# Optimization experiments

Hardware: AMD Instinct MI355X
Metric: run time of the kernel (lower is better)

The kernel has to match this reference:

```python
import jax, jax.numpy as jnp
import numpy as np
from jax import lax

B_SZ, N_CH, N_T = 512, 129, 250
D_MODEL = 128
D_INNER = 256            # expand * d_model
D_STATE = 16
D_CONV = 4
HEADDIM = 64             # mamba_ssm default
NHEADS = D_INNER // HEADDIM  # 4
CONV_DIM = D_INNER + 2 * D_STATE        # 288 (ngroups=1)
D_IN_PROJ = 2 * D_INNER + 2 * D_STATE + NHEADS  # 548
EPS = 1e-5


def setup_inputs() -> dict:
    key = jax.random.key(0)
    ks = jax.random.split(key, 12)
    g = lambda k, shp, s: jax.random.normal(k, shp, jnp.float32) * s
    dt0 = jax.random.uniform(ks[4], (NHEADS,), minval=0.001, maxval=0.1)
    return {
        "x": jax.random.normal(ks[0], (B_SZ, N_CH, N_T), jnp.float32),
        "mixer_w": g(ks[1], (D_MODEL, N_CH), 0.05),
        "mixer_b": jnp.zeros((D_MODEL,), jnp.float32),
        "in_proj_w": g(ks[2], (D_IN_PROJ, D_MODEL), 0.05),
        "conv_w": g(ks[3], (CONV_DIM, D_CONV), 0.2),
        "conv_b": jnp.zeros((CONV_DIM,), jnp.float32),
        "dt_bias": jnp.log(jnp.expm1(dt0)),               # inverse-softplus init
        "A_log": jnp.log(jax.random.uniform(ks[5], (NHEADS,), minval=1.0, maxval=16.0)),
        "D": jnp.ones((NHEADS,), jnp.float32),
        "norm_w": jnp.ones((D_INNER,), jnp.float32),
        "out_proj_w": g(ks[6], (D_MODEL, D_INNER), 0.05),
        "head_w": g(ks[7], (1, D_MODEL), 0.05),
        "head_b": jnp.zeros((1,), jnp.float32),
    }


def reference(x, mixer_w, mixer_b, in_proj_w, conv_w, conv_b, dt_bias,
              A_log, D, norm_w, out_proj_w, head_w, head_b):
    bsz, _, T = x.shape
    # channel mixer: (B, C, T) -> (B, T, d_model)
    u = jnp.einsum('bct,dc->btd', x, mixer_w) + mixer_b
    # Mamba2 in_proj (no bias)
    zxbcdt = u @ in_proj_w.T                        # (B, T, 548)
    z = zxbcdt[..., :D_INNER]                       # gate
    xBC = zxbcdt[..., D_INNER:D_INNER + CONV_DIM]   # (B, T, 288)
    dt = jax.nn.softplus(zxbcdt[..., -NHEADS:] + dt_bias)  # (B, T, H)
    # causal depthwise conv1d (kernel 4) + SiLU
    pad = jnp.pad(xBC, ((0, 0), (D_CONV - 1, 0), (0, 0)))
    xBC = sum(conv_w[:, k] * pad[:, k:k + T, :] for k in range(D_CONV)) + conv_b
    xBC = jax.nn.silu(xBC)
    xh = xBC[..., :D_INNER].reshape(bsz, T, NHEADS, HEADDIM)
    Bm = xBC[..., D_INNER:D_INNER + D_STATE]        # (B, T, N)
    Cm = xBC[..., D_INNER + D_STATE:]               # (B, T, N)
    A = -jnp.exp(A_log)                             # (H,)
    dA = jnp.exp(dt * A)                            # (B, T, H)
    # selective state-space scan, time-major
    tm = lambda a: jnp.moveaxis(a, 1, 0)
    def step(h, inp):
        dA_t, dt_t, x_t, B_t, C_t = inp
        # h: (B, H, P, N)
        h = h * dA_t[:, :, None, None] + (dt_t[..., None] * x_t)[..., None] * B_t[:, None, None, :]
        y_t = jnp.einsum('bhpn,bn->bhp', h, C_t)
        return h, y_t
    h0 = jnp.zeros((bsz, NHEADS, HEADDIM, D_STATE), x.dtype)
    _, ys = lax.scan(step, h0, (tm(dA), tm(dt), tm(xh), tm(Bm), tm(Cm)))
    y = jnp.moveaxis(ys, 0, 1) + D[:, None] * xh    # skip connection, (B, T, H, P)
    y = y.reshape(bsz, T, D_INNER)
    # gated RMSNorm (norm_before_gate=False)
    y = y * jax.nn.silu(z)
    y = y * lax.rsqrt(jnp.mean(y * y, axis=-1, keepdims=True) + EPS) * norm_w
    y = y @ out_proj_w.T                            # (B, T, d_model)
    # head: AdaptiveAvgPool1d(1) over time -> Flatten -> Linear(d_model, 1)
    pooled = jnp.mean(y, axis=1)                    # (B, d_model)
    return pooled @ head_w.T + head_b               # (B, 1)
```

## Files before the change

kernel.cpp:

```cpp
#include <hip/hip_runtime.h>
#include <math.h>

#define NCH     129
#define NT      250
#define DINNER  256
#define DSTATE  16
#define NHEADS  4
#define DPROJ   548
#define TC      8
#define MT      35
#define KS4     4
#define ZR      17
#define XK      136

typedef __attribute__((ext_vector_type(8))) short short8;
typedef __attribute__((ext_vector_type(4))) float f32x4;

template<int N> struct IC { static constexpr int value = N; };

__device__ __forceinline__ float silu_f(float x) { return x / (1.f + __expf(-x)); }

template<int CTRL>
__device__ __forceinline__ float dstep(float v) {
    int t = __builtin_amdgcn_update_dpp(0, __float_as_int(v), CTRL, 0xF, 0xF, true);
    return v + __int_as_float(t);
}
__device__ __forceinline__ float wave_sum63(float v) {
    v = dstep<0xB1>(v);  v = dstep<0x4E>(v);  v = dstep<0x141>(v);
    v = dstep<0x140>(v); v = dstep<0x142>(v); v = dstep<0x143>(v);
    return v;
}
__device__ __forceinline__ float rdlane(float v, int l) {
    return __uint_as_float(__builtin_amdgcn_readlane(__float_as_uint(v), l));
}
__device__ __forceinline__ unsigned short f2bf(float f) {
    unsigned u = __float_as_uint(f);
    u += 0x7FFF + ((u >> 16) & 1);
    return (unsigned short)(u >> 16);
}
__device__ __forceinline__ float bf2f(unsigned short h) {
    return __uint_as_float(((unsigned)h) << 16);
}

__global__ __launch_bounds__(256) void k_prep_w2(const float* __restrict__ in_proj_w,
                                                 const float* __restrict__ mixer_w,
                                                 const float* __restrict__ mixer_b,
                                                 float* __restrict__ w2t,
                                                 float* __restrict__ bias2) {
    int j = blockIdx.x;
    int c = threadIdx.x;
    if (c < NCH) {
        float acc = 0.f;
        for (int d = 0; d < 128; ++d)
            acc += in_proj_w[j * 128 + d] * mixer_w[d * NCH + c];
        w2t[(size_t)c * DPROJ + j] = acc;
    } else if (c == NCH) {
        float acc = 0.f;
        for (int d = 0; d < 128; ++d)
            acc += in_proj_w[j * 128 + d] * mixer_b[d];
        bias2[j] = acc;
    }
}

__global__ __launch_bounds__(256) void k_prep_v(const float* __restrict__ head_w,
                                                const float* __restrict__ out_proj_w,
                                                float* __restrict__ v) {
    int i = threadIdx.x;
    float acc = 0.f;
    for (int d = 0; d < 128; ++d)
        acc += head_w[d] * out_proj_w[(size_t)d * DINNER + i];
    v[i] = acc;
}

__global__ __launch_bounds__(64) void k_prep_frag(const float* __restrict__ w2t,
                                                  unsigned short* __restrict__ ahi,
                                                  unsigned short* __restrict__ alo) {
    int mt = blockIdx.x, ks = blockIdx.y;
    int lane = threadIdx.x;
    int m = mt * 16 + (lane & 15);
    size_t base = (((size_t)(mt * KS4 + ks)) * 64 + lane) * 8;
    for (int i = 0; i < 8; ++i) {
        int k = ks * 32 + (lane >> 4) * 8 + i;
        float v = (m < DPROJ) ? w2t[(size_t)k * DPROJ + m] : 0.f;
        unsigned short hb = f2bf(v);
        ahi[base + i] = hb;
        alo[base + i] = f2bf(v - bf2f(hb));
    }
}

__global__ __launch_bounds__(640, 2) void k_fused(
    const float* __restrict__ x,
    const unsigned short* __restrict__ ahi,
    const unsigned short* __restrict__ alo,
    const float* __restrict__ w2t,
    const float* __restrict__ bias2,
    const float* __restrict__ conv_w,
    const float* __restrict__ conv_b,
    const float* __restrict__ dt_bias,
    const float* __restrict__ A_log,
    const float* __restrict__ Dv,
    const float* __restrict__ norm_w,
    const float* __restrict__ vv,
    const float* __restrict__ head_b,
    float* __restrict__ out)
{
    __shared__ short xh[16 * XK];
    __shared__ short xl[16 * XK];
    __shared__ float x128buf[2][2][TC];
    __shared__ float zxbuf[DPROJ * ZR];
    __shared__ float bcbuf[2][TC][32];
    __shared__ float dtbuf[2][TC][NHEADS];
    __shared__ float dAbuf[2][TC][NHEADS];
    __shared__ float smp[2][2][TC][8];

    const int b2   = blockIdx.x;
    const int tid  = threadIdx.x;
    const int lane = tid & 63;
    const int wv   = tid >> 6;
    const bool isMain = (wv < 8);
    const int mb   = isMain ? (wv >> 2) : (wv - 8);
    const int p    = ((wv & 3) << 6) | lane;
    const int q    = lane;
    const int tcol = lane & 15;
    const int quad = lane >> 4;
    const bool isFold = isMain && ((wv & 3) == 0);

    const float* w128 = w2t + (size_t)128 * DPROJ;

    float bz = 0.f, bx = 0.f, w1z = 0.f, w1x = 0.f;
    float cw0 = 0.f, cw1 = 0.f, cw2 = 0.f, cw3 = 0.f, ccb = 0.f;
    float dtb = 0.f, Ah = 0.f, Dh = 0.f, nv = 0.f;
    if (isMain) {
        bz = bias2[p];          w1z = w128[p];
        bx = bias2[DINNER + p]; w1x = w128[DINNER + p];
        cw0 = conv_w[p * 4 + 0]; cw1 = conv_w[p * 4 + 1];
        cw2 = conv_w[p * 4 + 2]; cw3 = conv_w[p * 4 + 3];
        ccb = conv_b[p];
        Dh = Dv[p >> 6];
        nv = norm_w[p] * vv[p];
    } else if (q < 36) {
        bx  = bias2[2 * DINNER + q];
        w1x = w128[2 * DINNER + q];
        if (q < 32) {
            int ch = DINNER + q;
            cw0 = conv_w[ch * 4 + 0]; cw1 = conv_w[ch * 4 + 1];
            cw2 = conv_w[ch * 4 + 2]; cw3 = conv_w[ch * 4 + 3];
            ccb = conv_b[ch];
        } else {
            int h = q - 32;
            dtb = dt_bias[h];
            Ah  = -expf(A_log[h]);
        }
    }

    float za[TC], xa[TC], hs[DSTATE];
    float c1 = 0.f, c2 = 0.f, c3 = 0.f, outacc = 0.f;
#pragma unroll
    for (int n = 0; n < DSTATE; ++n) hs[n] = 0.f;

    const float* xb_aux = x + ((size_t)2 * b2 + mb) * NCH * NT;
    const int hh = wv & 3;
    float2 pr[9];

    auto load_chunk = [&](int t0, auto Lc) {
        constexpr int L  = decltype(Lc)::value;
        constexpr int HP = (L >= 2) ? L / 2 : 1;
        constexpr int PAIRS = NCH * HP;
#pragma unroll
        for (int k = 0; k * 64 < PAIRS; ++k) {
            int u = lane + 64 * k;
            if (u < PAIRS) {
                int c = u / HP, tp = u - c * HP;
                pr[k] = *(const float2*)(xb_aux + c * NT + t0 + 2 * tp);
            }
        }
    };
    auto store_chunk = [&](auto Lc, int nxtpar) {
        constexpr int L  = decltype(Lc)::value;
        constexpr int HP = (L >= 2) ? L / 2 : 1;
        constexpr int PAIRS = NCH * HP;
#pragma unroll
        for (int k = 0; k * 64 < PAIRS; ++k) {
            int u = lane + 64 * k;
            if (u < PAIRS) {
                int c = u / HP, tp = u - c * HP;
                float2 v = pr[k];
                if (c < 128) {
                    int row = mb * 8 + 2 * tp;
                    unsigned short h0 = f2bf(v.x), h1 = f2bf(v.y);
                    xh[row * XK + c]       = (short)h0;
                    xh[(row + 1) * XK + c] = (short)h1;
                    xl[row * XK + c]       = (short)f2bf(v.x - bf2f(h0));
                    xl[(row + 1) * XK + c] = (short)f2bf(v.y - bf2f(h1));
                } else {
                    x128buf[nxtpar][mb][2 * tp]     = v.x;
                    x128buf[nxtpar][mb][2 * tp + 1] = v.y;
                }
            }
        }
    };

    if (!isMain) { load_chunk(0, IC<TC>{}); store_chunk(IC<TC>{}, 0); }
    __syncthreads();

    auto stage = [&](auto CLc, auto NLc, int s) {
        constexpr int CL = decltype(CLc)::value;
        constexpr int NL = decltype(NLc)::value;
        const int cur = s & 1;

        if (isMain) {
            short8 bh[KS4], bl[KS4];
#pragma unroll
            for (int ks = 0; ks < KS4; ++ks) {
                bh[ks] = *(const short8*)&xh[tcol * XK + ks * 32 + quad * 8];
                bl[ks] = *(const short8*)&xl[tcol * XK + ks * 32 + quad * 8];
            }
            for (int mt = wv; mt < MT; mt += 8) {
                f32x4 a0 = {0.f, 0.f, 0.f, 0.f};
                f32x4 a1 = {0.f, 0.f, 0.f, 0.f};
#pragma unroll
                for (int ks = 0; ks < KS4; ++ks) {
                    size_t fo = (((size_t)(mt * KS4 + ks)) * 64 + lane) * 8;
                    short8 ah = *(const short8*)(ahi + fo);
                    short8 al = *(const short8*)(alo + fo);
                    a0 = __builtin_amdgcn_mfma_f32_16x16x32_bf16(ah, bh[ks], a0, 0, 0, 0);
                    a1 = __builtin_amdgcn_mfma_f32_16x16x32_bf16(ah, bl[ks], a1, 0, 0, 0);
                    a1 = __builtin_amdgcn_mfma_f32_16x16x32_bf16(al, bh[ks], a1, 0, 0, 0);
                }
#pragma unroll
                for (int r = 0; r < 4; ++r) {
                    int j = mt * 16 + quad * 4 + r;
                    if (j < DPROJ) zxbuf[j * ZR + tcol] = a0[r] + a1[r];
                }
            }
        } else {
            if constexpr (NL > 0) load_chunk((s + 1) * TC, IC<NL>{});
        }
        __syncthreads();

        if (isMain) {
            if (isFold && s > 0 && lane < TC) {
                const float* sp = smp[(s - 1) & 1][mb][lane];
                float s1 = sp[0] + sp[2] + sp[4] + sp[6];
                float s2 = sp[1] + sp[3] + sp[5] + sp[7];
                outacc = fmaf(s2, rsqrtf(fmaf(s1, 1.f / DINNER, 1e-5f)), outacc);
            }
#pragma unroll
            for (int tt = 0; tt < CL; ++tt) {
                float xm = x128buf[cur][mb][tt];
                int col = mb * 8 + tt;
                float zraw = zxbuf[p * ZR + col] + bz + w1z * xm;
                float xraw = zxbuf[(DINNER + p) * ZR + col] + bx + w1x * xm;
                float cv = fmaf(cw3, xraw, fmaf(cw2, c1, fmaf(cw1, c2, fmaf(cw0, c3, ccb))));
                c3 = c2; c2 = c1; c1 = xraw;
                xa[tt] = silu_f(cv);
                za[tt] = silu_f(zraw);
            }
        } else {
            if constexpr (NL > 0) store_chunk(IC<NL>{}, (s + 1) & 1);
            if (q < 32) {
#pragma unroll
                for (int tt = 0; tt < CL; ++tt) {
                    float xm = x128buf[cur][mb][tt];
                    float raw = zxbuf[(2 * DINNER + q) * ZR + mb * 8 + tt] + bx + w1x * xm;
                    float cv = fmaf(cw3, raw, fmaf(cw2, c1, fmaf(cw1, c2, fmaf(cw0, c3, ccb))));
                    c3 = c2; c2 = c1; c1 = raw;
                    bcbuf[mb][tt][q] = silu_f(cv);
                }
            } else if (q < 36) {
                int h = q - 32;
#pragma unroll
                for (int tt = 0; tt < CL; ++tt) {
                    float xm = x128buf[cur][mb][tt];
                    float val = zxbuf[(544 + h) * ZR + mb * 8 + tt] + bx + w1x * xm + dtb;
                    float dt = (val > 20.f) ? val : log1pf(expf(val));
                    dtbuf[mb][tt][h] = dt;
                    dAbuf[mb][tt][h] = __expf(dt * Ah);
                }
            }
        }
        __syncthreads();

        if (isMain) {
#pragma unroll
            for (int tt = 0; tt < CL; ++tt) {
                float xv  = xa[tt];
                float g   = za[tt];
                float dtv = dtbuf[mb][tt][hh];
                float dAv = dAbuf[mb][tt][hh];
                float bcv = bcbuf[mb][tt][lane & 31];
                float dx = dtv * xv;
                float y0 = 0.f, y1 = 0.f, y2 = 0.f, y3 = 0.f;
#pragma unroll
                for (int n = 0; n < 4; ++n) {
                    float b0 = rdlane(bcv, n),      cc0 = rdlane(bcv, DSTATE + n);
                    float b1 = rdlane(bcv, 4 + n),  cc1 = rdlane(bcv, DSTATE + 4 + n);
                    float b2v = rdlane(bcv, 8 + n), cc2 = rdlane(bcv, DSTATE + 8 + n);
                    float b3 = rdlane(bcv, 12 + n), cc3 = rdlane(bcv, DSTATE + 12 + n);
                    hs[n]      = fmaf(hs[n],      dAv, dx * b0);  y0 = fmaf(hs[n],      cc0, y0);
                    hs[4 + n]  = fmaf(hs[4 + n],  dAv, dx * b1);  y1 = fmaf(hs[4 + n],  cc1, y1);
                    hs[8 + n]  = fmaf(hs[8 + n],  dAv, dx * b2v); y2 = fmaf(hs[8 + n],  cc2, y2);
                    hs[12 + n] = fmaf(hs[12 + n], dAv, dx * b3);  y3 = fmaf(hs[12 + n], cc3, y3);
                }
                float val = fmaf(Dh, xv, (y0 + y1) + (y2 + y3)) * g;
                float s1 = wave_sum63(val * val);
                float s2 = wave_sum63(val * nv);
                if (lane == 63) {
                    smp[cur][mb][tt][2 * (wv & 3)]     = s1;
                    smp[cur][mb][tt][2 * (wv & 3) + 1] = s2;
                }
            }
        }
    };

    stage(IC<8>{}, IC<8>{}, 0);
    for (int s = 1; s <= 29; ++s) stage(IC<8>{}, IC<8>{}, s);
    stage(IC<8>{}, IC<2>{}, 30);
    stage(IC<2>{}, IC<0>{}, 31);
    __syncthreads();

    if (isFold) {
        if (lane < 2) {
            const float* sp = smp[1][mb][lane];
            float s1 = sp[0] + sp[2] + sp[4] + sp[6];
            float s2 = sp[1] + sp[3] + sp[5] + sp[7];
            outacc = fmaf(s2, rsqrtf(fmaf(s1, 1.f / DINNER, 1e-5f)), outacc);
        }
        float tot = wave_sum63(outacc);
        if (lane == 63) out[2 * b2 + mb] = head_b[0] + tot * (1.f / NT);
    }
}

extern "C" void kernel_launch(void* const* d_in, const int* in_sizes, int n_in,
                              void* d_out, int out_size, void* d_ws, size_t ws_size,
                              hipStream_t stream) {
    const float* x         = (const float*)d_in[0];
    const float* mixer_w   = (const float*)d_in[1];
    const float* mixer_b   = (const float*)d_in[2];
    const float* in_proj_w = (const float*)d_in[3];
    const float* conv_w    = (const float*)d_in[4];
    const float* conv_b    = (const float*)d_in[5];
    const float* dt_bias   = (const float*)d_in[6];
    const float* A_log     = (const float*)d_in[7];
    const float* Dp        = (const float*)d_in[8];
    const float* norm_w    = (const float*)d_in[9];
    const float* out_proj_w= (const float*)d_in[10];
    const float* head_w    = (const float*)d_in[11];
    const float* head_b    = (const float*)d_in[12];
    float* out = (float*)d_out;

    int B = in_sizes[0] / (NCH * NT);

    float* ws    = (float*)d_ws;
    float* w2t   = ws;
    float* bias2 = w2t + (size_t)NCH * DPROJ;
    float* vvp   = bias2 + DPROJ;
    unsigned short* ahi = (unsigned short*)(vvp + DINNER);
    unsigned short* alo = ahi + (size_t)MT * KS4 * 64 * 8;

    k_prep_w2<<<DPROJ, 256, 0, stream>>>(in_proj_w, mixer_w, mixer_b, w2t, bias2);
    k_prep_v<<<1, 256, 0, stream>>>(head_w, out_proj_w, vvp);
    k_prep_frag<<<dim3(MT, KS4), 64, 0, stream>>>(w2t, ahi, alo);
    k_fused<<<B / 2, 640, 0, stream>>>(x, ahi, alo, w2t, bias2, conv_w, conv_b,
                                       dt_bias, A_log, Dp, norm_w, vvp, head_b, out);
}
```

Before: 428.4 us.

## Use one batch per block with 16-step time chunks and prefetched A fragments

Each block now handles one batch element with 5 waves (4 main, 1 loader) instead of two batch elements with 10 waves. The time chunk doubles to 16 steps, so all 16 MFMA columns hold real timesteps and there are half as many stage barriers. The A-fragment loads are double-buffered across M-tiles to hide global latency. In exchange there are twice as many blocks and more registers per thread (larger prefetch arrays and buffered fragments), which may limit occupancy.

```diff
diff --git a/kernel.cpp b/kernel.cpp
--- a/kernel.cpp
+++ b/kernel.cpp
@@ -7,7 +7,7 @@
 #define DSTATE  16
 #define NHEADS  4
 #define DPROJ   548
-#define TC      8
+#define TC      16
 #define MT      35
 #define KS4     4
 #define ZR      17
@@ -88,7 +88,7 @@
     }
 }
 
-__global__ __launch_bounds__(640, 2) void k_fused(
+__global__ __launch_bounds__(320, 3) void k_fused(
     const float* __restrict__ x,
     const unsigned short* __restrict__ ahi,
     const unsigned short* __restrict__ alo,
@@ -104,26 +104,25 @@
     const float* __restrict__ head_b,
     float* __restrict__ out)
 {
-    __shared__ short xh[16 * XK];
-    __shared__ short xl[16 * XK];
-    __shared__ float x128buf[2][2][TC];
+    __shared__ short xh[TC * XK];
+    __shared__ short xl[TC * XK];
+    __shared__ float x128buf[2][TC];
     __shared__ float zxbuf[DPROJ * ZR];
-    __shared__ float bcbuf[2][TC][32];
-    __shared__ float dtbuf[2][TC][NHEADS];
-    __shared__ float dAbuf[2][TC][NHEADS];
-    __shared__ float smp[2][2][TC][8];
-
-    const int b2   = blockIdx.x;
+    __shared__ float bcbuf[TC][32];
+    __shared__ float dtbuf[TC][NHEADS];
+    __shared__ float dAbuf[TC][NHEADS];
+    __shared__ float smp[2][TC][8];
+
+    const int b    = blockIdx.x;
     const int tid  = threadIdx.x;
     const int lane = tid & 63;
     const int wv   = tid >> 6;
-    const bool isMain = (wv < 8);
-    const int mb   = isMain ? (wv >> 2) : (wv - 8);
-    const int p    = ((wv & 3) << 6) | lane;
+    const bool isMain = (wv < 4);
+    const int p    = (wv << 6) | lane;
     const int q    = lane;
     const int tcol = lane & 15;
     const int quad = lane >> 4;
-    const bool isFold = isMain && ((wv & 3) == 0);
+    const bool isFold = (wv == 0);
 
     const float* w128 = w2t + (size_t)128 * DPROJ;
 
@@ -136,7 +135,7 @@
         cw0 = conv_w[p * 4 + 0]; cw1 = conv_w[p * 4 + 1];
         cw2 = conv_w[p * 4 + 2]; cw3 = conv_w[p * 4 + 3];
         ccb = conv_b[p];
-        Dh = Dv[p >> 6];
+        Dh = Dv[wv];
         nv = norm_w[p] * vv[p];
     } else if (q < 36) {
         bx  = bias2[2 * DINNER + q];
@@ -158,9 +157,8 @@
 #pragma unroll
     for (int n = 0; n < DSTATE; ++n) hs[n] = 0.f;
 
-    const float* xb_aux = x + ((size_t)2 * b2 + mb) * NCH * NT;
-    const int hh = wv & 3;
-    float2 pr[9];
+    const float* xb = x + (size_t)b * NCH * NT;
+    float2 pr[17];
 
     auto load_chunk = [&](int t0, auto Lc) {
         constexpr int L  = decltype(Lc)::value;
@@ -171,7 +169,7 @@
             int u = lane + 64 * k;
             if (u < PAIRS) {
                 int c = u / HP, tp = u - c * HP;
-                pr[k] = *(const float2*)(xb_aux + c * NT + t0 + 2 * tp);
+                pr[k] = *(const float2*)(xb + c * NT + t0 + 2 * tp);
             }
         }
     };
@@ -186,15 +184,15 @@
                 int c = u / HP, tp = u - c * HP;
                 float2 v = pr[k];
                 if (c < 128) {
-                    int row = mb * 8 + 2 * tp;
+                    int row = 2 * tp;
                     unsigned short h0 = f2bf(v.x), h1 = f2bf(v.y);
                     xh[row * XK + c]       = (short)h0;
                     xh[(row + 1) * XK + c] = (short)h1;
                     xl[row * XK + c]       = (short)f2bf(v.x - bf2f(h0));
                     xl[(row + 1) * XK + c] = (short)f2bf(v.y - bf2f(h1));
                 } else {
-                    x128buf[nxtpar][mb][2 * tp]     = v.x;
-                    x128buf[nxtpar][mb][2 * tp + 1] = v.y;
+                    x128buf[nxtpar][2 * tp]     = v.x;
+                    x128buf[nxtpar][2 * tp + 1] = v.y;
                 }
             }
         }
@@ -215,23 +213,41 @@
                 bh[ks] = *(const short8*)&xh[tcol * XK + ks * 32 + quad * 8];
                 bl[ks] = *(const short8*)&xl[tcol * XK + ks * 32 + quad * 8];
             }
-            for (int mt = wv; mt < MT; mt += 8) {
+            short8 f0h[KS4], f0l[KS4], f1h[KS4], f1l[KS4];
+            auto loadA = [&](int mt, short8 (&fh)[KS4], short8 (&fl)[KS4]) {
+#pragma unroll
+                for (int ks = 0; ks < KS4; ++ks) {
+                    size_t fo = (((size_t)(mt * KS4 + ks)) * 64 + lane) * 8;
+                    fh[ks] = *(const short8*)(ahi + fo);
+                    fl[ks] = *(const short8*)(alo + fo);
+                }
+            };
+            auto tileC = [&](int mt, short8 (&fh)[KS4], short8 (&fl)[KS4]) {
                 f32x4 a0 = {0.f, 0.f, 0.f, 0.f};
                 f32x4 a1 = {0.f, 0.f, 0.f, 0.f};
 #pragma unroll
                 for (int ks = 0; ks < KS4; ++ks) {
-                    size_t fo = (((size_t)(mt * KS4 + ks)) * 64 + lane) * 8;
-                    short8 ah = *(const short8*)(ahi + fo);
-                    short8 al = *(const short8*)(alo + fo);
-                    a0 = __builtin_amdgcn_mfma_f32_16x16x32_bf16(ah, bh[ks], a0, 0, 0, 0);
-                    a1 = __builtin_amdgcn_mfma_f32_16x16x32_bf16(ah, bl[ks], a1, 0, 0, 0);
-                    a1 = __builtin_amdgcn_mfma_f32_16x16x32_bf16(al, bh[ks], a1, 0, 0, 0);
+                    a0 = __builtin_amdgcn_mfma_f32_16x16x32_bf16(fh[ks], bh[ks], a0, 0, 0, 0);
+                    a1 = __builtin_amdgcn_mfma_f32_16x16x32_bf16(fh[ks], bl[ks], a1, 0, 0, 0);
+                    a1 = __builtin_amdgcn_mfma_f32_16x16x32_bf16(fl[ks], bh[ks], a1, 0, 0, 0);
                 }
 #pragma unroll
                 for (int r = 0; r < 4; ++r) {
                     int j = mt * 16 + quad * 4 + r;
                     if (j < DPROJ) zxbuf[j * ZR + tcol] = a0[r] + a1[r];
                 }
+            };
+            int mt = wv;
+            loadA(mt, f0h, f0l);
+            while (true) {
+                if (mt + 4 < MT) loadA(mt + 4, f1h, f1l);
+                tileC(mt, f0h, f0l);
+                mt += 4;
+                if (mt >= MT) break;
+                if (mt + 4 < MT) loadA(mt + 4, f0h, f0l);
+                tileC(mt, f1h, f1l);
+                mt += 4;
+                if (mt >= MT) break;
             }
         } else {
             if constexpr (NL > 0) load_chunk((s + 1) * TC, IC<NL>{});
@@ -240,17 +256,16 @@
 
         if (isMain) {
             if (isFold && s > 0 && lane < TC) {
-                const float* sp = smp[(s - 1) & 1][mb][lane];
+                const float* sp = smp[(s - 1) & 1][lane];
                 float s1 = sp[0] + sp[2] + sp[4] + sp[6];
                 float s2 = sp[1] + sp[3] + sp[5] + sp[7];
                 outacc = fmaf(s2, rsqrtf(fmaf(s1, 1.f / DINNER, 1e-5f)), outacc);
             }
 #pragma unroll
             for (int tt = 0; tt < CL; ++tt) {
-                float xm = x128buf[cur][mb][tt];
-                int col = mb * 8 + tt;
-                float zraw = zxbuf[p * ZR + col] + bz + w1z * xm;
-                float xraw = zxbuf[(DINNER + p) * ZR + col] + bx + w1x * xm;
+                float xm = x128buf[cur][tt];
+                float zraw = zxbuf[p * ZR + tt] + bz + w1z * xm;
+                float xraw = zxbuf[(DINNER + p) * ZR + tt] + bx + w1x * xm;
                 float cv = fmaf(cw3, xraw, fmaf(cw2, c1, fmaf(cw1, c2, fmaf(cw0, c3, ccb))));
                 c3 = c2; c2 = c1; c1 = xraw;
                 xa[tt] = silu_f(cv);
@@ -261,21 +276,21 @@
             if (q < 32) {
 #pragma unroll
                 for (int tt = 0; tt < CL; ++tt) {
-                    float xm = x128buf[cur][mb][tt];
-                    float raw = zxbuf[(2 * DINNER + q) * ZR + mb * 8 + tt] + bx + w1x * xm;
+                    float xm = x128buf[cur][tt];
+                    float raw = zxbuf[(2 * DINNER + q) * ZR + tt] + bx + w1x * xm;
                     float cv = fmaf(cw3, raw, fmaf(cw2, c1, fmaf(cw1, c2, fmaf(cw0, c3, ccb))));
                     c3 = c2; c2 = c1; c1 = raw;
-                    bcbuf[mb][tt][q] = silu_f(cv);
+                    bcbuf[tt][q] = silu_f(cv);
                 }
             } else if (q < 36) {
                 int h = q - 32;
 #pragma unroll
                 for (int tt = 0; tt < CL; ++tt) {
-                    float xm = x128buf[cur][mb][tt];
-                    float val = zxbuf[(544 + h) * ZR + mb * 8 + tt] + bx + w1x * xm + dtb;
+                    float xm = x128buf[cur][tt];
+                    float val = zxbuf[(544 + h) * ZR + tt] + bx + w1x * xm + dtb;
                     float dt = (val > 20.f) ? val : log1pf(expf(val));
-                    dtbuf[mb][tt][h] = dt;
-                    dAbuf[mb][tt][h] = __expf(dt * Ah);
+                    dtbuf[tt][h] = dt;
+                    dAbuf[tt][h] = __expf(dt * Ah);
                 }
             }
         }
@@ -286,9 +301,9 @@
             for (int tt = 0; tt < CL; ++tt) {
                 float xv  = xa[tt];
                 float g   = za[tt];
-                float dtv = dtbuf[mb][tt][hh];
-                float dAv = dAbuf[mb][tt][hh];
-                float bcv = bcbuf[mb][tt][lane & 31];
+                float dtv = dtbuf[tt][wv];
+                float dAv = dAbuf[tt][wv];
+                float bcv = bcbuf[tt][lane & 31];
                 float dx = dtv * xv;
                 float y0 = 0.f, y1 = 0.f, y2 = 0.f, y3 = 0.f;
 #pragma unroll
@@ -306,28 +321,28 @@
                 float s1 = wave_sum63(val * val);
                 float s2 = wave_sum63(val * nv);
                 if (lane == 63) {
-                    smp[cur][mb][tt][2 * (wv & 3)]     = s1;
-                    smp[cur][mb][tt][2 * (wv & 3) + 1] = s2;
+                    smp[cur][tt][2 * wv]     = s1;
+                    smp[cur][tt][2 * wv + 1] = s2;
                 }
             }
         }
     };
 
-    stage(IC<8>{}, IC<8>{}, 0);
-    for (int s = 1; s <= 29; ++s) stage(IC<8>{}, IC<8>{}, s);
-    stage(IC<8>{}, IC<2>{}, 30);
-    stage(IC<2>{}, IC<0>{}, 31);
+#pragma unroll 1
+    for (int s = 0; s <= 13; ++s) stage(IC<16>{}, IC<16>{}, s);
+    stage(IC<16>{}, IC<10>{}, 14);
+    stage(IC<10>{}, IC<0>{}, 15);
     __syncthreads();
 
     if (isFold) {
-        if (lane < 2) {
-            const float* sp = smp[1][mb][lane];
+        if (lane < 10) {
+            const float* sp = smp[1][lane];
             float s1 = sp[0] + sp[2] + sp[4] + sp[6];
             float s2 = sp[1] + sp[3] + sp[5] + sp[7];
             outacc = fmaf(s2, rsqrtf(fmaf(s1, 1.f / DINNER, 1e-5f)), outacc);
         }
         float tot = wave_sum63(outacc);
-        if (lane == 63) out[2 * b2 + mb] = head_b[0] + tot * (1.f / NT);
+        if (lane == 63) out[b] = head_b[0] + tot * (1.f / NT);
     }
 }
 
@@ -361,6 +376,6 @@
     k_prep_w2<<<DPROJ, 256, 0, stream>>>(in_proj_w, mixer_w, mixer_b, w2t, bias2);
     k_prep_v<<<1, 256, 0, stream>>>(head_w, out_proj_w, vvp);
     k_prep_frag<<<dim3(MT, KS4), 64, 0, stream>>>(w2t, ahi, alo);
-    k_fused<<<B / 2, 640, 0, stream>>>(x, ahi, alo, w2t, bias2, conv_w, conv_b,
-                                       dt_bias, A_log, Dp, norm_w, vvp, head_b, out);
-}
+    k_fused<<<B, 320, 0, stream>>>(x, ahi, alo, w2t, bias2, conv_w, conv_b,
+                                   dt_bias, A_log, Dp, norm_w, vvp, head_b, out);
+}
```

New measurement: 913.3 us. 113% more time.

## Double time chunk to 16 and add helper waves for loading

Applied to the files above, without the earlier changes.

Each stage now processes 16 timesteps instead of 8, so every weight fragment loaded from global memory feeds two MFMA column tiles and the number of stages and barriers is halved. Two extra helper waves are added (768 threads), splitting the x-chunk loading between halves. The cost is more registers and shared memory per block, and the launch bound asks for 3 blocks per CU with 768 threads, which may force register spills. The final fold now handles the 10-step tail.

```diff
diff --git a/kernel.cpp b/kernel.cpp
--- a/kernel.cpp
+++ b/kernel.cpp
@@ -7,10 +7,10 @@
 #define DSTATE  16
 #define NHEADS  4
 #define DPROJ   548
-#define TC      8
+#define TC      16
 #define MT      35
 #define KS4     4
-#define ZR      17
+#define ZR      33
 #define XK      136
 
 typedef __attribute__((ext_vector_type(8))) short short8;
@@ -88,7 +88,7 @@
     }
 }
 
-__global__ __launch_bounds__(640, 2) void k_fused(
+__global__ __launch_bounds__(768, 3) void k_fused(
     const float* __restrict__ x,
     const unsigned short* __restrict__ ahi,
     const unsigned short* __restrict__ alo,
@@ -104,8 +104,8 @@
     const float* __restrict__ head_b,
     float* __restrict__ out)
 {
-    __shared__ short xh[16 * XK];
-    __shared__ short xl[16 * XK];
+    __shared__ short xh[32 * XK];
+    __shared__ short xl[32 * XK];
     __shared__ float x128buf[2][2][TC];
     __shared__ float zxbuf[DPROJ * ZR];
     __shared__ float bcbuf[2][TC][32];
@@ -118,7 +118,8 @@
     const int lane = tid & 63;
     const int wv   = tid >> 6;
     const bool isMain = (wv < 8);
-    const int mb   = isMain ? (wv >> 2) : (wv - 8);
+    const int mb   = isMain ? (wv >> 2) : ((wv - 8) >> 1);
+    const int hf   = isMain ? 0 : ((wv - 8) & 1);
     const int p    = ((wv & 3) << 6) | lane;
     const int q    = lane;
     const int tcol = lane & 15;
@@ -136,7 +137,7 @@
         cw0 = conv_w[p * 4 + 0]; cw1 = conv_w[p * 4 + 1];
         cw2 = conv_w[p * 4 + 2]; cw3 = conv_w[p * 4 + 3];
         ccb = conv_b[p];
-        Dh = Dv[p >> 6];
+        Dh = Dv[wv & 3];
         nv = norm_w[p] * vv[p];
     } else if (q < 36) {
         bx  = bias2[2 * DINNER + q];
@@ -186,55 +187,68 @@
                 int c = u / HP, tp = u - c * HP;
                 float2 v = pr[k];
                 if (c < 128) {
-                    int row = mb * 8 + 2 * tp;
+                    int row = mb * 16 + hf * 8 + 2 * tp;
                     unsigned short h0 = f2bf(v.x), h1 = f2bf(v.y);
                     xh[row * XK + c]       = (short)h0;
                     xh[(row + 1) * XK + c] = (short)h1;
                     xl[row * XK + c]       = (short)f2bf(v.x - bf2f(h0));
                     xl[(row + 1) * XK + c] = (short)f2bf(v.y - bf2f(h1));
                 } else {
-                    x128buf[nxtpar][mb][2 * tp]     = v.x;
-                    x128buf[nxtpar][mb][2 * tp + 1] = v.y;
+                    x128buf[nxtpar][mb][hf * 8 + 2 * tp]     = v.x;
+                    x128buf[nxtpar][mb][hf * 8 + 2 * tp + 1] = v.y;
                 }
             }
         }
     };
 
-    if (!isMain) { load_chunk(0, IC<TC>{}); store_chunk(IC<TC>{}, 0); }
+    if (!isMain) { load_chunk(hf * 8, IC<8>{}); store_chunk(IC<8>{}, 0); }
     __syncthreads();
 
     auto stage = [&](auto CLc, auto NLc, int s) {
         constexpr int CL = decltype(CLc)::value;
         constexpr int NL = decltype(NLc)::value;
+        constexpr int NL0 = (NL > 8) ? 8 : NL;
+        constexpr int NL1 = (NL > 8) ? NL - 8 : 0;
         const int cur = s & 1;
 
         if (isMain) {
-            short8 bh[KS4], bl[KS4];
+            short8 bh0[KS4], bl0[KS4], bh1[KS4], bl1[KS4];
 #pragma unroll
             for (int ks = 0; ks < KS4; ++ks) {
-                bh[ks] = *(const short8*)&xh[tcol * XK + ks * 32 + quad * 8];
-                bl[ks] = *(const short8*)&xl[tcol * XK + ks * 32 + quad * 8];
+                bh0[ks] = *(const short8*)&xh[tcol * XK + ks * 32 + quad * 8];
+                bl0[ks] = *(const short8*)&xl[tcol * XK + ks * 32 + quad * 8];
+                bh1[ks] = *(const short8*)&xh[(16 + tcol) * XK + ks * 32 + quad * 8];
+                bl1[ks] = *(const short8*)&xl[(16 + tcol) * XK + ks * 32 + quad * 8];
             }
             for (int mt = wv; mt < MT; mt += 8) {
-                f32x4 a0 = {0.f, 0.f, 0.f, 0.f};
-                f32x4 a1 = {0.f, 0.f, 0.f, 0.f};
+                f32x4 a00 = {0.f, 0.f, 0.f, 0.f};
+                f32x4 a01 = {0.f, 0.f, 0.f, 0.f};
+                f32x4 a10 = {0.f, 0.f, 0.f, 0.f};
+                f32x4 a11 = {0.f, 0.f, 0.f, 0.f};
 #pragma unroll
                 for (int ks = 0; ks < KS4; ++ks) {
                     size_t fo = (((size_t)(mt * KS4 + ks)) * 64 + lane) * 8;
                     short8 ah = *(const short8*)(ahi + fo);
                     short8 al = *(const short8*)(alo + fo);
-                    a0 = __builtin_amdgcn_mfma_f32_16x16x32_bf16(ah, bh[ks], a0, 0, 0, 0);
-                    a1 = __builtin_amdgcn_mfma_f32_16x16x32_bf16(ah, bl[ks], a1, 0, 0, 0);
-                    a1 = __builtin_amdgcn_mfma_f32_16x16x32_bf16(al, bh[ks], a1, 0, 0, 0);
+                    a00 = __builtin_amdgcn_mfma_f32_16x16x32_bf16(ah, bh0[ks], a00, 0, 0, 0);
+                    a01 = __builtin_amdgcn_mfma_f32_16x16x32_bf16(ah, bl0[ks], a01, 0, 0, 0);
+                    a01 = __builtin_amdgcn_mfma_f32_16x16x32_bf16(al, bh0[ks], a01, 0, 0, 0);
+                    a10 = __builtin_amdgcn_mfma_f32_16x16x32_bf16(ah, bh1[ks], a10, 0, 0, 0);
+                    a11 = __builtin_amdgcn_mfma_f32_16x16x32_bf16(ah, bl1[ks], a11, 0, 0, 0);
+                    a11 = __builtin_amdgcn_mfma_f32_16x16x32_bf16(al, bh1[ks], a11, 0, 0, 0);
                 }
 #pragma unroll
                 for (int r = 0; r < 4; ++r) {
                     int j = mt * 16 + quad * 4 + r;
-                    if (j < DPROJ) zxbuf[j * ZR + tcol] = a0[r] + a1[r];
+                    if (j < DPROJ) {
+                        zxbuf[j * ZR + tcol]      = a00[r] + a01[r];
+                        zxbuf[j * ZR + 16 + tcol] = a10[r] + a11[r];
+                    }
                 }
             }
         } else {
-            if constexpr (NL > 0) load_chunk((s + 1) * TC, IC<NL>{});
+            if (hf == 0) { if constexpr (NL0 > 0) load_chunk((s + 1) * TC,     IC<NL0>{}); }
+            else         { if constexpr (NL1 > 0) load_chunk((s + 1) * TC + 8, IC<NL1>{}); }
         }
         __syncthreads();
 
@@ -248,7 +262,7 @@
 #pragma unroll
             for (int tt = 0; tt < CL; ++tt) {
                 float xm = x128buf[cur][mb][tt];
-                int col = mb * 8 + tt;
+                int col = mb * 16 + tt;
                 float zraw = zxbuf[p * ZR + col] + bz + w1z * xm;
                 float xraw = zxbuf[(DINNER + p) * ZR + col] + bx + w1x * xm;
                 float cv = fmaf(cw3, xraw, fmaf(cw2, c1, fmaf(cw1, c2, fmaf(cw0, c3, ccb))));
@@ -257,25 +271,28 @@
                 za[tt] = silu_f(zraw);
             }
         } else {
-            if constexpr (NL > 0) store_chunk(IC<NL>{}, (s + 1) & 1);
-            if (q < 32) {
-#pragma unroll
-                for (int tt = 0; tt < CL; ++tt) {
-                    float xm = x128buf[cur][mb][tt];
-                    float raw = zxbuf[(2 * DINNER + q) * ZR + mb * 8 + tt] + bx + w1x * xm;
-                    float cv = fmaf(cw3, raw, fmaf(cw2, c1, fmaf(cw1, c2, fmaf(cw0, c3, ccb))));
-                    c3 = c2; c2 = c1; c1 = raw;
-                    bcbuf[mb][tt][q] = silu_f(cv);
-                }
-            } else if (q < 36) {
-                int h = q - 32;
-#pragma unroll
-                for (int tt = 0; tt < CL; ++tt) {
-                    float xm = x128buf[cur][mb][tt];
-                    float val = zxbuf[(544 + h) * ZR + mb * 8 + tt] + bx + w1x * xm + dtb;
-                    float dt = (val > 20.f) ? val : log1pf(expf(val));
-                    dtbuf[mb][tt][h] = dt;
-                    dAbuf[mb][tt][h] = __expf(dt * Ah);
+            if (hf == 0) { if constexpr (NL0 > 0) store_chunk(IC<NL0>{}, (s + 1) & 1); }
+            else         { if constexpr (NL1 > 0) store_chunk(IC<NL1>{}, (s + 1) & 1); }
+            if (hf == 0) {
+                if (q < 32) {
+#pragma unroll
+                    for (int tt = 0; tt < CL; ++tt) {
+                        float xm = x128buf[cur][mb][tt];
+                        float raw = zxbuf[(2 * DINNER + q) * ZR + mb * 16 + tt] + bx + w1x * xm;
+                        float cv = fmaf(cw3, raw, fmaf(cw2, c1, fmaf(cw1, c2, fmaf(cw0, c3, ccb))));
+                        c3 = c2; c2 = c1; c1 = raw;
+                        bcbuf[mb][tt][q] = silu_f(cv);
+                    }
+                } else if (q < 36) {
+                    int h = q - 32;
+#pragma unroll
+                    for (int tt = 0; tt < CL; ++tt) {
+                        float xm = x128buf[cur][mb][tt];
+                        float val = zxbuf[(544 + h) * ZR + mb * 16 + tt] + bx + w1x * xm + dtb;
+                        float dt = (val > 20.f) ? val : log1pf(expf(val));
+                        dtbuf[mb][tt][h] = dt;
+                        dAbuf[mb][tt][h] = __expf(dt * Ah);
+                    }
                 }
             }
         }
@@ -313,14 +330,14 @@
         }
     };
 
-    stage(IC<8>{}, IC<8>{}, 0);
-    for (int s = 1; s <= 29; ++s) stage(IC<8>{}, IC<8>{}, s);
-    stage(IC<8>{}, IC<2>{}, 30);
-    stage(IC<2>{}, IC<0>{}, 31);
+#pragma unroll 1
+    for (int s = 0; s <= 13; ++s) stage(IC<16>{}, IC<16>{}, s);
+    stage(IC<16>{}, IC<10>{}, 14);
+    stage(IC<10>{}, IC<0>{}, 15);
     __syncthreads();
 
     if (isFold) {
-        if (lane < 2) {
+        if (lane < 10) {
             const float* sp = smp[1][mb][lane];
             float s1 = sp[0] + sp[2] + sp[4] + sp[6];
             float s2 = sp[1] + sp[3] + sp[5] + sp[7];
@@ -361,6 +378,6 @@
     k_prep_w2<<<DPROJ, 256, 0, stream>>>(in_proj_w, mixer_w, mixer_b, w2t, bias2);
     k_prep_v<<<1, 256, 0, stream>>>(head_w, out_proj_w, vvp);
     k_prep_frag<<<dim3(MT, KS4), 64, 0, stream>>>(w2t, ahi, alo);
-    k_fused<<<B / 2, 640, 0, stream>>>(x, ahi, alo, w2t, bias2, conv_w, conv_b,
+    k_fused<<<B / 2, 768, 0, stream>>>(x, ahi, alo, w2t, bias2, conv_w, conv_b,
                                        dt_bias, A_log, Dp, norm_w, vvp, head_b, out);
 }
```

After: 609.9 us. +42.4%, slower.

## Split fused kernel into parallel MFMA GEMM kernel and per-batch scan kernel

Applied to the files above, without the earlier changes.

Splits the fused projection-plus-scan kernel into two. The first is a GEMM kernel tiled over batch and 32-step time blocks that writes the full in_proj output to a workspace buffer. The second is a scan kernel with one block per batch that streams those rows, applying conv, SiLU, the SSM recurrence, gated RMSNorm and the folded head. This exposes more parallelism for the GEMM and removes it from the serial scan's critical path, at the cost of a large global round-trip (B*250*560 floats). It falls back to the fused kernel when the workspace is too small.

```diff
diff --git a/kernel.cpp b/kernel.cpp
--- a/kernel.cpp
+++ b/kernel.cpp
@@ -12,6 +12,8 @@
 #define KS4     4
 #define ZR      17
 #define XK      136
+#define ZXR     560
+#define GZR     33
 
 typedef __attribute__((ext_vector_type(8))) short short8;
 typedef __attribute__((ext_vector_type(4))) float f32x4;
@@ -85,6 +87,241 @@
         unsigned short hb = f2bf(v);
         ahi[base + i] = hb;
         alo[base + i] = f2bf(v - bf2f(hb));
+    }
+}
+
+__global__ __launch_bounds__(512, 2) void k_gemm(
+    const float* __restrict__ x,
+    const unsigned short* __restrict__ ahi,
+    const unsigned short* __restrict__ alo,
+    float* __restrict__ zx)
+{
+    __shared__ short xh[32 * XK];
+    __shared__ short xl[32 * XK];
+    __shared__ float zxb[288 * GZR];
+
+    const int b   = blockIdx.x;
+    const int t0  = blockIdx.y * 32;
+    const int TV  = (NT - t0 < 32) ? (NT - t0) : 32;
+    const int tid = threadIdx.x;
+    const int lane = tid & 63;
+    const int wv   = tid >> 6;
+    const int tcol = lane & 15;
+    const int quad = lane >> 4;
+
+    const float* xb = x + (size_t)b * NCH * NT;
+
+    auto stg = [&](auto HPc) {
+        constexpr int HP = decltype(HPc)::value;
+        constexpr int PAIRS = 128 * HP;
+#pragma unroll
+        for (int k = 0; k * 512 < PAIRS; ++k) {
+            int u = tid + 512 * k;
+            if (u < PAIRS) {
+                int c = u / HP, tp = u - c * HP;
+                float2 v = *(const float2*)(xb + c * NT + t0 + 2 * tp);
+                int row = 2 * tp;
+                unsigned short h0 = f2bf(v.x), h1 = f2bf(v.y);
+                xh[row * XK + c]       = (short)h0;
+                xh[(row + 1) * XK + c] = (short)h1;
+                xl[row * XK + c]       = (short)f2bf(v.x - bf2f(h0));
+                xl[(row + 1) * XK + c] = (short)f2bf(v.y - bf2f(h1));
+            }
+        }
+    };
+    if (TV == 32) stg(IC<16>{}); else stg(IC<13>{});
+    __syncthreads();
+
+    float* orow = zx + ((size_t)b * NT + t0) * ZXR;
+
+    auto gemm_half = [&](int mt0, int mt1, int rbase) {
+        for (int mt = mt0 + wv; mt < mt1; mt += 8) {
+            size_t fo = (((size_t)(mt * KS4)) * 64 + lane) * 8;
+            const unsigned short* ap = ahi + fo;
+            const unsigned short* lp = alo + fo;
+            short8 A0 = *(const short8*)(ap);
+            short8 A1 = *(const short8*)(ap + 512);
+            short8 A2 = *(const short8*)(ap + 1024);
+            short8 A3 = *(const short8*)(ap + 1536);
+            short8 L0 = *(const short8*)(lp);
+            short8 L1 = *(const short8*)(lp + 512);
+            short8 L2 = *(const short8*)(lp + 1024);
+            short8 L3 = *(const short8*)(lp + 1536);
+            f32x4 a0 = {0.f, 0.f, 0.f, 0.f};
+            f32x4 a1 = {0.f, 0.f, 0.f, 0.f};
+#pragma unroll
+            for (int ks = 0; ks < KS4; ++ks) {
+                short8 Ak = (ks == 0) ? A0 : (ks == 1) ? A1 : (ks == 2) ? A2 : A3;
+                short8 Lk = (ks == 0) ? L0 : (ks == 1) ? L1 : (ks == 2) ? L2 : L3;
+                short8 bh = *(const short8*)&xh[tcol * XK + ks * 32 + quad * 8];
+                short8 bl = *(const short8*)&xl[tcol * XK + ks * 32 + quad * 8];
+                a0 = __builtin_amdgcn_mfma_f32_16x16x32_bf16(Ak, bh, a0, 0, 0, 0);
+                a0 = __builtin_amdgcn_mfma_f32_16x16x32_bf16(Ak, bl, a0, 0, 0, 0);
+                a0 = __builtin_amdgcn_mfma_f32_16x16x32_bf16(Lk, bh, a0, 0, 0, 0);
+            }
+#pragma unroll
+            for (int ks = 0; ks < KS4; ++ks) {
+                short8 Ak = (ks == 0) ? A0 : (ks == 1) ? A1 : (ks == 2) ? A2 : A3;
+                short8 Lk = (ks == 0) ? L0 : (ks == 1) ? L1 : (ks == 2) ? L2 : L3;
+                short8 bh = *(const short8*)&xh[(16 + tcol) * XK + ks * 32 + quad * 8];
+                short8 bl = *(const short8*)&xl[(16 + tcol) * XK + ks * 32 + quad * 8];
+                a1 = __builtin_amdgcn_mfma_f32_16x16x32_bf16(Ak, bh, a1, 0, 0, 0);
+                a1 = __builtin_amdgcn_mfma_f32_16x16x32_bf16(Ak, bl, a1, 0, 0, 0);
+                a1 = __builtin_amdgcn_mfma_f32_16x16x32_bf16(Lk, bh, a1, 0, 0, 0);
+            }
+#pragma unroll
+            for (int r = 0; r < 4; ++r) {
+                int j = mt * 16 + quad * 4 + r;
+                if (j < DPROJ) {
+                    int lr = j - rbase;
+                    zxb[lr * GZR + tcol]      = a0[r];
+                    zxb[lr * GZR + 16 + tcol] = a1[r];
+                }
+            }
+        }
+    };
+
+    gemm_half(0, 18, 0);
+    __syncthreads();
+    for (int idx = tid; idx < 288 * TV; idx += 512) {
+        int t = idx / 288, j = idx - t * 288;
+        orow[(size_t)t * ZXR + j] = zxb[j * GZR + t];
+    }
+    __syncthreads();
+    gemm_half(18, 35, 288);
+    __syncthreads();
+    for (int idx = tid; idx < 260 * TV; idx += 512) {
+        int t = idx / 260, jj = idx - t * 260;
+        orow[(size_t)t * ZXR + 288 + jj] = zxb[jj * GZR + t];
+    }
+}
+
+__global__ __launch_bounds__(256, 4) void k_scan(
+    const float* __restrict__ zx,
+    const float* __restrict__ x,
+    const float* __restrict__ w2t,
+    const float* __restrict__ bias2,
+    const float* __restrict__ conv_w,
+    const float* __restrict__ conv_b,
+    const float* __restrict__ dt_bias,
+    const float* __restrict__ A_log,
+    const float* __restrict__ Dv,
+    const float* __restrict__ norm_w,
+    const float* __restrict__ vv,
+    const float* __restrict__ head_b,
+    float* __restrict__ out)
+{
+    __shared__ float smp[2][16][4][2];
+
+    const int b    = blockIdx.x;
+    const int tid  = threadIdx.x;
+    const int lane = tid & 63;
+    const int h    = tid >> 6;
+
+    const float* w128 = w2t + (size_t)128 * DPROJ;
+    const int p = 64 * h + lane;
+
+    const float bz  = bias2[p],           w1z = w128[p];
+    const float bx  = bias2[DINNER + p],  w1x = w128[DINNER + p];
+    const float cw0 = conv_w[p * 4 + 0], cw1 = conv_w[p * 4 + 1];
+    const float cw2 = conv_w[p * 4 + 2], cw3 = conv_w[p * 4 + 3];
+    const float ccb = conv_b[p];
+    const float Dh  = Dv[h];
+    const float nv  = norm_w[p] * vv[p];
+    float bx2 = 0.f, w1x2 = 0.f, dw0 = 0.f, dw1 = 0.f, dw2 = 0.f, dw3 = 0.f, dcb = 0.f;
+    if (lane < 32) {
+        int q = lane, ch = DINNER + q;
+        bx2  = bias2[2 * DINNER + q];
+        w1x2 = w128[2 * DINNER + q];
+        dw0 = conv_w[ch * 4 + 0]; dw1 = conv_w[ch * 4 + 1];
+        dw2 = conv_w[ch * 4 + 2]; dw3 = conv_w[ch * 4 + 3];
+        dcb = conv_b[ch];
+    }
+    const float bdt = bias2[544 + h], wdt = w128[544 + h];
+    const float dtb = dt_bias[h];
+    const float Ah  = -expf(A_log[h]);
+
+    float hs[DSTATE];
+#pragma unroll
+    for (int n = 0; n < DSTATE; ++n) hs[n] = 0.f;
+    float c1 = 0.f, c2 = 0.f, c3 = 0.f;
+    float d1 = 0.f, d2 = 0.f, d3 = 0.f;
+    float outacc = 0.f;
+
+    const float* zrow = zx + (size_t)b * NT * ZXR;
+    const float* xmp  = x + ((size_t)b * NCH + 128) * NT;
+
+    float pz  = zrow[p];
+    float px  = zrow[256 + p];
+    float pbc = (lane < 32) ? zrow[512 + lane] : 0.f;
+    float pdt = zrow[544 + h];
+    float pxm = xmp[0];
+
+    int t = 0;
+    for (int s = 0; s < 16; ++s) {
+        const int CL  = (s < 15) ? 16 : 10;
+        const int par = s & 1;
+        for (int tt = 0; tt < CL; ++tt, ++t) {
+            float nz = 0.f, nx = 0.f, nbc = 0.f, ndt = 0.f, nxm = 0.f;
+            if (t + 1 < NT) {
+                const float* r = zrow + (size_t)(t + 1) * ZXR;
+                nz  = r[p];
+                nx  = r[256 + p];
+                nbc = (lane < 32) ? r[512 + lane] : 0.f;
+                ndt = r[544 + h];
+                nxm = xmp[t + 1];
+            }
+            const float xm = pxm;
+            const float g  = silu_f(pz + bz + w1z * xm);
+            const float xraw = px + bx + w1x * xm;
+            float cv = fmaf(cw3, xraw, fmaf(cw2, c1, fmaf(cw1, c2, fmaf(cw0, c3, ccb))));
+            c3 = c2; c2 = c1; c1 = xraw;
+            const float xa = silu_f(cv);
+            float bcs;
+            {
+                float r2  = pbc + bx2 + w1x2 * xm;
+                float cv2 = fmaf(dw3, r2, fmaf(dw2, d1, fmaf(dw1, d2, fmaf(dw0, d3, dcb))));
+                d3 = d2; d2 = d1; d1 = r2;
+                bcs = silu_f(cv2);
+            }
+            float dval = pdt + bdt + wdt * xm + dtb;
+            float dtv  = (dval > 20.f) ? dval : log1pf(expf(dval));
+            float dAv  = __expf(dtv * Ah);
+            float dx   = dtv * xa;
+
+            float y0 = 0.f, y1 = 0.f, y2 = 0.f, y3 = 0.f;
+#pragma unroll
+            for (int n = 0; n < 4; ++n) {
+                float b0  = rdlane(bcs, n),      cc0 = rdlane(bcs, DSTATE + n);
+                float b1v = rdlane(bcs, 4 + n),  cc1 = rdlane(bcs, DSTATE + 4 + n);
+                float b2v = rdlane(bcs, 8 + n),  cc2 = rdlane(bcs, DSTATE + 8 + n);
+                float b3v = rdlane(bcs, 12 + n), cc3 = rdlane(bcs, DSTATE + 12 + n);
+                hs[n]      = fmaf(hs[n],      dAv, dx * b0);  y0 = fmaf(hs[n],      cc0, y0);
+                hs[4 + n]  = fmaf(hs[4 + n],  dAv, dx * b1v); y1 = fmaf(hs[4 + n],  cc1, y1);
+                hs[8 + n]  = fmaf(hs[8 + n],  dAv, dx * b2v); y2 = fmaf(hs[8 + n],  cc2, y2);
+                hs[12 + n] = fmaf(hs[12 + n], dAv, dx * b3v); y3 = fmaf(hs[12 + n], cc3, y3);
+            }
+            float val = fmaf(Dh, xa, (y0 + y1) + (y2 + y3)) * g;
+            float s1 = wave_sum63(val * val);
+            float s2 = wave_sum63(val * nv);
+            if (lane == 63) {
+                smp[par][tt][h][0] = s1;
+                smp[par][tt][h][1] = s2;
+            }
+            pz = nz; px = nx; pbc = nbc; pdt = ndt; pxm = nxm;
+        }
+        __syncthreads();
+        if (h == 0 && lane < CL) {
+            float t1 = (smp[par][lane][0][0] + smp[par][lane][1][0]) +
+                       (smp[par][lane][2][0] + smp[par][lane][3][0]);
+            float t2 = (smp[par][lane][0][1] + smp[par][lane][1][1]) +
+                       (smp[par][lane][2][1] + smp[par][lane][3][1]);
+            outacc = fmaf(t2, rsqrtf(fmaf(t1, 1.f / DINNER, 1e-5f)), outacc);
+        }
+    }
+    if (h == 0) {
+        float tot = wave_sum63(outacc);
+        if (lane == 63) out[b] = head_b[0] + tot * (1.f / NT);
     }
 }
 
@@ -358,9 +595,22 @@
     unsigned short* ahi = (unsigned short*)(vvp + DINNER);
     unsigned short* alo = ahi + (size_t)MT * KS4 * 64 * 8;
 
+    size_t prep_end = (size_t)((char*)(alo + (size_t)MT * KS4 * 64 * 8) - (char*)d_ws);
+    size_t zx_off   = (prep_end + 255) & ~(size_t)255;
+    size_t need     = zx_off + (size_t)B * NT * ZXR * sizeof(float);
+
     k_prep_w2<<<DPROJ, 256, 0, stream>>>(in_proj_w, mixer_w, mixer_b, w2t, bias2);
     k_prep_v<<<1, 256, 0, stream>>>(head_w, out_proj_w, vvp);
     k_prep_frag<<<dim3(MT, KS4), 64, 0, stream>>>(w2t, ahi, alo);
-    k_fused<<<B / 2, 640, 0, stream>>>(x, ahi, alo, w2t, bias2, conv_w, conv_b,
-                                       dt_bias, A_log, Dp, norm_w, vvp, head_b, out);
-}
+
+    if (ws_size >= need) {
+        float* zx = (float*)((char*)d_ws + zx_off);
+        int ntiles = (NT + 31) / 32;
+        k_gemm<<<dim3(B, ntiles), 512, 0, stream>>>(x, ahi, alo, zx);
+        k_scan<<<B, 256, 0, stream>>>(zx, x, w2t, bias2, conv_w, conv_b, dt_bias,
+                                      A_log, Dp, norm_w, vvp, head_b, out);
+    } else {
+        k_fused<<<B / 2, 640, 0, stream>>>(x, ahi, alo, w2t, bias2, conv_w, conv_b,
+                                           dt_bias, A_log, Dp, norm_w, vvp, head_b, out);
+    }
+}
```

Measured after the change: 431.2 us. About the same (+0.7%).
